# Optimization experiments

Measured on AMD Instinct MI355X. Metric: run time of the kernel, lower is better.

## Reference

```python
import jax, jax.numpy as jnp
import numpy as np

HIDDEN = 896
N_HEADS = 14
N_KV = 2
HEAD_DIM = 64
GROUPS = N_HEADS // N_KV  # 7
ROPE_THETA = 1000000.0
B, S = 2, 2048
NEG = -1e9


def rotate_half(x):
    x1 = x[..., : x.shape[-1] // 2]
    x2 = x[..., x.shape[-1] // 2:]
    return jnp.concatenate([-x2, x1], axis=-1)


def setup_inputs() -> dict:
    key = jax.random.key(0)
    ks = jax.random.split(key, 8)
    scale = 0.02
    hidden_states = jax.random.normal(ks[0], (B, S, HIDDEN), dtype=jnp.float32)
    # causal additive mask [1,1,S,S]
    causal = jnp.tril(jnp.ones((S, S), dtype=bool))
    attention_mask = jnp.where(causal, 0.0, NEG).astype(jnp.float32)[None, None]
    Wq = jax.random.normal(ks[1], (HIDDEN, N_HEADS * HEAD_DIM), dtype=jnp.float32) * scale
    bq = jnp.zeros((N_HEADS * HEAD_DIM,), dtype=jnp.float32)
    Wk = jax.random.normal(ks[2], (HIDDEN, N_KV * HEAD_DIM), dtype=jnp.float32) * scale
    bk = jnp.zeros((N_KV * HEAD_DIM,), dtype=jnp.float32)
    Wv = jax.random.normal(ks[3], (HIDDEN, N_KV * HEAD_DIM), dtype=jnp.float32) * scale
    bv = jnp.zeros((N_KV * HEAD_DIM,), dtype=jnp.float32)
    Wo = jax.random.normal(ks[4], (HIDDEN, HIDDEN), dtype=jnp.float32) * scale
    return {"hidden_states": hidden_states, "attention_mask": attention_mask,
            "Wq": Wq, "bq": bq, "Wk": Wk, "bk": bk, "Wv": Wv, "bv": bv,
            "Wo": Wo, "position_offset": 0}


def reference(hidden_states, attention_mask, Wq, bq, Wk, bk, Wv, bv, Wo, position_offset):
    batch, seq, _ = hidden_states.shape
    # QKV projections -> [B, heads, S, head_dim]
    q = (hidden_states @ Wq + bq).reshape(batch, seq, N_HEADS, HEAD_DIM).transpose(0, 2, 1, 3)
    k = (hidden_states @ Wk + bk).reshape(batch, seq, N_KV, HEAD_DIM).transpose(0, 2, 1, 3)
    v = (hidden_states @ Wv + bv).reshape(batch, seq, N_KV, HEAD_DIM).transpose(0, 2, 1, 3)
    # RoPE (computed inline from position_offset, matches precomputed cos/sin tables)
    inv_freq = 1.0 / (ROPE_THETA ** (jnp.arange(0, HEAD_DIM, 2, dtype=jnp.float32) / HEAD_DIM))
    pos = (position_offset + jnp.arange(seq)).astype(jnp.float32)  # [S]
    freqs = pos[:, None] * inv_freq[None, :]  # [S, HD/2]
    emb = jnp.concatenate([freqs, freqs], axis=-1)  # [S, HD]
    cos = jnp.cos(emb)[None, None]  # [1,1,S,HD]
    sin = jnp.sin(emb)[None, None]
    q = q * cos + rotate_half(q) * sin
    k = k * cos + rotate_half(k) * sin
    # GQA: repeat kv heads
    k = jnp.repeat(k, GROUPS, axis=1)
    v = jnp.repeat(v, GROUPS, axis=1)
    scores = jnp.einsum('bhqd,bhkd->bhqk', q, k) / jnp.sqrt(jnp.float32(HEAD_DIM))
    scores = scores + attention_mask
    weights = jax.nn.softmax(scores, axis=-1)
    out = jnp.einsum('bhqk,bhkd->bhqd', weights, v)
    out = out.transpose(0, 2, 1, 3).reshape(batch, seq, HIDDEN)
    return out @ Wo
```

## Files before the change

kernel.cpp:

```cpp
#include <hip/hip_runtime.h>
#include <stdint.h>

#define DEV __device__ __forceinline__

using bf16x8 = __attribute__((ext_vector_type(8))) short;
using f32x4  = __attribute__((ext_vector_type(4))) float;

DEV float b2f(uint16_t h){ return __uint_as_float(((uint32_t)h)<<16); }
DEV uint16_t f2b(float f){ uint32_t u=__float_as_uint(f); u += 0x7fffu + ((u>>16)&1u); return (uint16_t)(u>>16); }
DEV uint32_t pk2(float a, float b){
  return __builtin_amdgcn_perm(__float_as_uint(b), __float_as_uint(a), 0x07060302u);
}

#define GLOAD16(gp, lp) __builtin_amdgcn_global_load_lds( \
    (__attribute__((address_space(1))) void*)(gp), \
    (__attribute__((address_space(3))) void*)(lp), 16, 0, 0)

constexpr int S_    = 2048;
constexpr int HID   = 896;
constexpr int NH    = 14;
constexpr int NKV   = 2;
constexpr int HD    = 64;
constexpr int BATCH = 2;
constexpr int MROWS = BATCH * S_;
constexpr int NQKV  = 1152;
constexpr int SROWS = 1536;
constexpr int OPSTR = BATCH * NH * SROWS * 64;
constexpr int MLSTR = BATCH * NH * SROWS;
constexpr float QSCALE = 0.125f * 1.4426950408889634f;

__global__ void prep_all_kernel(const float* __restrict__ X,
                                const float* __restrict__ Wq, const float* __restrict__ Wk,
                                const float* __restrict__ Wv, const float* __restrict__ Wo,
                                const float* __restrict__ bq, const float* __restrict__ bk,
                                const float* __restrict__ bv, const int* __restrict__ pos0,
                                uint16_t* __restrict__ Xb,
                                uint16_t* __restrict__ WqkvT, uint16_t* __restrict__ WoT,
                                float* __restrict__ bqkv,
                                float* __restrict__ cosT, float* __restrict__ sinT) {
  const int blk = blockIdx.x, tid = threadIdx.x;
  if (blk < 1792) {
    const int lx = tid & 31, ly = tid >> 5;
    const float* src; uint16_t* dst; int ncols, rowOff, i;
    if (blk < 784)       { src = Wq; dst = WqkvT; ncols = 896; rowOff = 0;    i = blk;       }
    else if (blk < 896)  { src = Wk; dst = WqkvT; ncols = 128; rowOff = 896;  i = blk - 784; }
    else if (blk < 1008) { src = Wv; dst = WqkvT; ncols = 128; rowOff = 1024; i = blk - 896; }
    else                 { src = Wo; dst = WoT;   ncols = 896; rowOff = 0;    i = blk - 1008;}
    const int nb = ncols >> 5;
    const int n0 = (i % nb) * 32, k0 = (i / nb) * 32;
    __shared__ uint16_t tile[32][33];
    #pragma unroll
    for (int r = 0; r < 32; r += 8)
      tile[ly + r][lx] = f2b(src[(size_t)(k0 + ly + r) * ncols + (n0 + lx)]);
    __syncthreads();
    #pragma unroll
    for (int r = 0; r < 32; r += 8)
      dst[(size_t)(rowOff + n0 + ly + r) * 896 + (k0 + lx)] = tile[lx][ly + r];
  } else if (blk < 5376) {
    int i = (blk - 1792) * 256 + tid;
    float4 v = ((const float4*)X)[i];
    union { uint16_t u[4]; uint64_t q; } r;
    r.u[0] = f2b(v.x); r.u[1] = f2b(v.y); r.u[2] = f2b(v.z); r.u[3] = f2b(v.w);
    ((uint64_t*)Xb)[i] = r.q;
  } else if (blk < 5632) {
    int idx = (blk - 5376) * 256 + tid;
    int s = idx >> 5, j = idx & 31;
    float inv = exp2f(-(float)j * (19.931568569324174f / 32.0f));
    float ang = (float)(pos0[0] + s) * inv;
    float sv, cv;
    sincosf(ang, &sv, &cv);
    cosT[idx] = cv; sinT[idx] = sv;
  } else {
    int i = (blk - 5632) * 256 + tid;
    if (i < NQKV) bqkv[i] = i < 896 ? bq[i] : (i < 1024 ? bk[i - 896] : bv[i - 1024]);
  }
}

__global__ void packv_kernel(const uint16_t* __restrict__ Vf, uint16_t* __restrict__ Vt) {
  __shared__ uint16_t tile[64][65];
  const int s0 = blockIdx.x * 64;
  const int g  = blockIdx.y;
  const int b = g >> 1, kv = g & 1;
  const int lx = threadIdx.x & 63, ly = threadIdx.x >> 6;
  #pragma unroll
  for (int i = 0; i < 64; i += 4)
    tile[ly + i][lx] = Vf[(size_t)(b * S_ + s0 + ly + i) * 128 + kv * 64 + lx];
  __syncthreads();
  #pragma unroll
  for (int i = 0; i < 64; i += 4)
    Vt[((size_t)g * HD + ly + i) * S_ + s0 + lx] = tile[lx][ly + i];
}

template <int EPI>
__global__ __launch_bounds__(256) void gemm_bt_kernel(
    const uint16_t* __restrict__ A, const uint16_t* __restrict__ Bt,
    const float* __restrict__ bias, void* __restrict__ Cv, int N, int K,
    const float* __restrict__ cosT, const float* __restrict__ sinT,
    uint16_t* __restrict__ Qb, uint16_t* __restrict__ Kb, uint16_t* __restrict__ Vf) {
  __shared__ __align__(16) uint16_t As[128 * 64];
  __shared__ __align__(16) uint16_t Bs[64 * 64];
  const int tid = threadIdx.x;
  const int l = tid & 63, w = tid >> 6;
  const int m0 = blockIdx.x * 128, n0 = blockIdx.y * 64;
  const int wr = w * 32;

  f32x4 acc[2][4] = {};
  for (int k0 = 0; k0 < K; k0 += 64) {
    #pragma unroll
    for (int i = 0; i < 4; ++i) {
      int cid = i * 256 + tid;
      int row = cid >> 3;
      int sch = (cid & 7) ^ (row & 7);
      GLOAD16(A + (size_t)(m0 + row) * K + (k0 + sch * 8), (char*)As + cid * 16);
    }
    #pragma unroll
    for (int i = 0; i < 2; ++i) {
      int cid = i * 256 + tid;
      int row = cid >> 3;
      int sch = (cid & 7) ^ (row & 7);
      GLOAD16(Bt + (size_t)(n0 + row) * K + (k0 + sch * 8), (char*)Bs + cid * 16);
    }
    __syncthreads();
    __builtin_amdgcn_s_setprio(1);
    #pragma unroll
    for (int ks = 0; ks < 2; ++ks) {
      bf16x8 af[2], bfr[4];
      #pragma unroll
      for (int mi = 0; mi < 2; ++mi) {
        int row = wr + mi * 16 + (l & 15);
        int ch = ((l >> 4) + ks * 4) ^ (row & 7);
        af[mi] = *(const bf16x8*)((const char*)As + row * 128 + ch * 16);
      }
      #pragma unroll
      for (int ni = 0; ni < 4; ++ni) {
        int row = ni * 16 + (l & 15);
        int ch = ((l >> 4) + ks * 4) ^ (row & 7);
        bfr[ni] = *(const bf16x8*)((const char*)Bs + row * 128 + ch * 16);
      }
      #pragma unroll
      for (int mi = 0; mi < 2; ++mi)
        #pragma unroll
        for (int ni = 0; ni < 4; ++ni)
          acc[mi][ni] = __builtin_amdgcn_mfma_f32_16x16x32_bf16(af[mi], bfr[ni], acc[mi][ni], 0, 0, 0);
    }
    __builtin_amdgcn_s_setprio(0);
    __syncthreads();
  }

  const int tc = l & 15, g = l >> 4;
  if (EPI == 1) {
    if (n0 < 896) {
      #pragma unroll
      for (int mi = 0; mi < 2; ++mi) {
        #pragma unroll
        for (int jr = 0; jr < 4; ++jr) {
          int row = m0 + wr + mi * 16 + g * 4 + jr;
          int bb = row >> 11, s = row & (S_ - 1);
          const float* cp = cosT + s * 32;
          const float* sp = sinT + s * 32;
          #pragma unroll
          for (int ni = 0; ni < 2; ++ni) {
            int col = n0 + ni * 16 + tc;
            int j = col & 63;
            float c = cp[j], sn = sp[j];
            float alo = acc[mi][ni][jr] + bias[col];
            float ahi = acc[mi][ni + 2][jr] + bias[col + 32];
            size_t dst = ((size_t)(bb * NH + (n0 >> 6)) * S_ + s) * HD + j;
            Qb[dst]      = f2b((alo * c - ahi * sn) * QSCALE);
            Qb[dst + 32] = f2b((ahi * c + alo * sn) * QSCALE);
          }
        }
      }
    } else if (n0 < 1024) {
      #pragma unroll
      for (int mi = 0; mi < 2; ++mi) {
        #pragma unroll
        for (int jr = 0; jr < 4; ++jr) {
          int row = m0 + wr + mi * 16 + g * 4 + jr;
          int bb = row >> 11, s = row & (S_ - 1);
          const float* cp = cosT + s * 32;
          const float* sp = sinT + s * 32;
          #pragma unroll
          for (int ni = 0; ni < 2; ++ni) {
            int col = n0 + ni * 16 + tc;
            int j = col & 63;
            float c = cp[j], sn = sp[j];
            float alo = acc[mi][ni][jr] + bias[col];
            float ahi = acc[mi][ni + 2][jr] + bias[col + 32];
            size_t dst = ((size_t)(bb * NKV + ((n0 - 896) >> 6)) * S_ + s) * HD + j;
            Kb[dst]      = f2b(alo * c - ahi * sn);
            Kb[dst + 32] = f2b(ahi * c + alo * sn);
          }
        }
      }
    } else {
      #pragma unroll
      for (int mi = 0; mi < 2; ++mi)
        #pragma unroll
        for (int ni = 0; ni < 4; ++ni) {
          int col = n0 + ni * 16 + tc;
          #pragma unroll
          for (int jr = 0; jr < 4; ++jr) {
            int row = m0 + wr + mi * 16 + g * 4 + jr;
            Vf[(size_t)row * 128 + (col - 1024)] = f2b(acc[mi][ni][jr] + bias[col]);
          }
        }
    }
  } else {
    #pragma unroll
    for (int mi = 0; mi < 2; ++mi) {
      #pragma unroll
      for (int ni = 0; ni < 4; ++ni) {
        int col = n0 + ni * 16 + tc;
        #pragma unroll
        for (int j = 0; j < 4; ++j) {
          int row = m0 + wr + mi * 16 + g * 4 + j;
          ((float*)Cv)[(size_t)row * N + col] = acc[mi][ni][j];
        }
      }
    }
  }
}

__global__ __launch_bounds__(448) void attn_kernel(
    const uint16_t* __restrict__ Qb, const uint16_t* __restrict__ Kb,
    const uint16_t* __restrict__ Vt, uint16_t* __restrict__ Ob,
    uint16_t* __restrict__ Op, float2* __restrict__ mlp) {
  __shared__ __align__(16) uint16_t Ks[2][64 * 64];
  __shared__ __align__(16) uint16_t Vs[2][64 * 64];
  const int tid = threadIdx.x, l = tid & 63, w = tid >> 6;
  const int u = blockIdx.x;
  const int kv = blockIdx.y & 1, b = blockIdx.y >> 1;
  const int tc = l & 15, g = l >> 4;
  const int srcA = (((2 * g) & 3) << 4) | tc;
  const int srcB = (((2 * g + 1) & 3) << 4) | tc;

  int qt16, ck;
  if (u < 32)       { qt16 = u;                   ck = 0; }
  else if (u < 96)  { int i = u - 32;  qt16 = 32 + (i >> 1); ck = i & 1; }
  else if (u < 192) { int i = u - 96;  int q3 = i / 3; qt16 = 64 + q3; ck = i - 3 * q3; }
  else              { int i = u - 192; qt16 = 96 + (i >> 2); ck = i & 3; }
  const int ntiles = (qt16 >> 2) + 1;
  const int nch    = (qt16 >> 5) + 1;
  const int tlo    = 8 * ck;
  const int thi    = (8 * ck + 8 < ntiles) ? (8 * ck + 8) : ntiles;
  const int ns     = thi - tlo;
  const bool dodiag = (ck == nch - 1);
  const bool split  = (nch > 1);

  const int h  = kv * 7 + w;
  const int qg = qt16 * 16 + tc;

  const uint16_t* Khead = Kb + (size_t)(b * NKV + kv) * S_ * HD;
  const uint16_t* Vhead = Vt + (size_t)(b * NKV + kv) * HD * S_;

  auto stage = [&](int t, int bi) {
    const int t0 = t * 64;
    #pragma unroll
    for (int i = 0; i < 2; ++i) {
      if (i == 0 || tid < 64) {
        int cid = i * 448 + tid;
        int row = cid >> 3, sch = (cid & 7) ^ (row & 7);
        GLOAD16(Khead + (size_t)(t0 + row) * HD + sch * 8, (char*)Ks[bi] + cid * 16);
        GLOAD16(Vhead + (size_t)row * S_ + t0 + sch * 8,   (char*)Vs[bi] + cid * 16);
      }
    }
  };

  const uint16_t* qptr = Qb + ((size_t)(b * NH + h) * S_ + qg) * HD + g * 8;
  bf16x8 qf0 = *(const bf16x8*)qptr;
  bf16x8 qf1 = *(const bf16x8*)(qptr + 32);

  f32x4 oacc[4] = {};
  float mrow = -1e30f, lrow = 0.f;

  stage(tlo, 0);

  #pragma unroll 1
  for (int i = 0; i < ns; ++i) {
    const int t = tlo + i;
    asm volatile("s_waitcnt vmcnt(0)" ::: "memory");
    __builtin_amdgcn_s_barrier();
    if (i + 1 < ns) stage(t + 1, (i + 1) & 1);

    const uint16_t* Kc = Ks[i & 1];
    const uint16_t* Vc = Vs[i & 1];
    const int t0 = t * 64;

    f32x4 sacc[4] = {};
    __builtin_amdgcn_s_setprio(1);
    #pragma unroll
    for (int ks = 0; ks < 2; ++ks) {
      bf16x8 qf = ks ? qf1 : qf0;
      #pragma unroll
      for (int c = 0; c < 4; ++c) {
        int trow = c * 16 + tc;
        int ch = (g + ks * 4) ^ (tc & 7);
        bf16x8 kf = *(const bf16x8*)((const char*)Kc + trow * 128 + ch * 16);
        sacc[c] = __builtin_amdgcn_mfma_f32_16x16x32_bf16(kf, qf, sacc[c], 0, 0, 0);
      }
    }
    __builtin_amdgcn_s_setprio(0);

    if (dodiag && t == ntiles - 1) {
      #pragma unroll
      for (int c = 0; c < 4; ++c) {
        int kvb = t0 + c * 16 + g * 4;
        #pragma unroll
        for (int r = 0; r < 4; ++r)
          if (kvb + r > qg) sacc[c][r] = -1e30f;
      }
    }

    float pmax = sacc[0][0];
    #pragma unroll
    for (int c = 0; c < 4; ++c)
      #pragma unroll
      for (int r = 0; r < 4; ++r) pmax = fmaxf(pmax, sacc[c][r]);
    if (__any(pmax > mrow + 11.5f)) {
      float mt = fmaxf(pmax, __shfl_xor(pmax, 16));
      mt = fmaxf(mt, __shfl_xor(mt, 32));
      float mn = fmaxf(mrow, mt);
      float corr = exp2f(mrow - mn);
      mrow = mn;
      lrow *= corr;
      #pragma unroll
      for (int dt = 0; dt < 4; ++dt) oacc[dt] *= corr;
    }
    float rs = 0.f;
    #pragma unroll
    for (int c = 0; c < 4; ++c)
      #pragma unroll
      for (int r = 0; r < 4; ++r) {
        float e = exp2f(sacc[c][r] - mrow);
        sacc[c][r] = e; rs += e;
      }
    lrow += rs;

    uint32_t w0[4], w1[4];
    #pragma unroll
    for (int c = 0; c < 4; ++c) {
      w0[c] = pk2(sacc[c][0], sacc[c][1]);
      w1[c] = pk2(sacc[c][2], sacc[c][3]);
    }
    const bool lo = g < 2;
    bf16x8 pf[2];
    {
      union { uint32_t u[4]; bf16x8 v; } p0, p1;
      uint32_t a0 = __shfl((int)w0[0], srcA), a1 = __shfl((int)w1[0], srcA);
      uint32_t a2 = __shfl((int)w0[0], srcB), a3 = __shfl((int)w1[0], srcB);
      uint32_t b0 = __shfl((int)w0[1], srcA), b1 = __shfl((int)w1[1], srcA);
      uint32_t b2 = __shfl((int)w0[1], srcB), b3 = __shfl((int)w1[1], srcB);
      p0.u[0] = lo ? a0 : b0; p0.u[1] = lo ? a1 : b1;
      p0.u[2] = lo ? a2 : b2; p0.u[3] = lo ? a3 : b3;
      pf[0] = p0.v;
      uint32_t c0 = __shfl((int)w0[2], srcA), c1 = __shfl((int)w1[2], srcA);
      uint32_t c2 = __shfl((int)w0[2], srcB), c3 = __shfl((int)w1[2], srcB);
      uint32_t d0 = __shfl((int)w0[3], srcA), d1 = __shfl((int)w1[3], srcA);
      uint32_t d2 = __shfl((int)w0[3], srcB), d3 = __shfl((int)w1[3], srcB);
      p1.u[0] = lo ? c0 : d0; p1.u[1] = lo ? c1 : d1;
      p1.u[2] = lo ? c2 : d2; p1.u[3] = lo ? c3 : d3;
      pf[1] = p1.v;
    }

    __builtin_amdgcn_s_setprio(1);
    #pragma unroll
    for (int ks = 0; ks < 2; ++ks) {
      #pragma unroll
      for (int dt = 0; dt < 4; ++dt) {
        int drow = dt * 16 + tc;
        int vch = (g + ks * 4) ^ (tc & 7);
        bf16x8 vf = *(const bf16x8*)((const char*)Vc + drow * 128 + vch * 16);
        oacc[dt] = __builtin_amdgcn_mfma_f32_16x16x32_bf16(vf, pf[ks], oacc[dt], 0, 0, 0);
      }
    }
    __builtin_amdgcn_s_setprio(0);
  }

  float ltot = lrow;
  ltot += __shfl_xor(ltot, 16);
  ltot += __shfl_xor(ltot, 32);

  if (!split) {
    float inv = 1.0f / ltot;
    size_t obase = (size_t)(b * S_ + qg) * HID + h * HD;
    #pragma unroll
    for (int dt = 0; dt < 4; ++dt) {
      union { uint16_t u[4]; uint64_t q; } o;
      #pragma unroll
      for (int r = 0; r < 4; ++r) o.u[r] = f2b(oacc[dt][r] * inv);
      *(uint64_t*)(Ob + obase + dt * 16 + g * 4) = o.q;
    }
  } else {
    size_t rowid = (size_t)(b * NH + h) * SROWS + (qg - 512);
    uint16_t* Opc = Op + (size_t)ck * OPSTR + rowid * 64;
    #pragma unroll
    for (int dt = 0; dt < 4; ++dt) {
      union { uint16_t u[4]; uint64_t q; } o;
      #pragma unroll
      for (int r = 0; r < 4; ++r) o.u[r] = f2b(oacc[dt][r]);
      *(uint64_t*)(Opc + dt * 16 + g * 4) = o.q;
    }
    if (g == 0) mlp[(size_t)ck * MLSTR + rowid] = make_float2(mrow, ltot);
  }
}

__global__ void combine_kernel(const uint16_t* __restrict__ Op, const float2* __restrict__ mlp,
                               uint16_t* __restrict__ Ob) {
  int idx = blockIdx.x * 256 + threadIdx.x;
  int r = idx >> 4;
  int d0 = (idx & 15) * 4;
  int bh = r / SROWS;
  int sr = r - bh * SROWS;
  int s = 512 + sr;
  int nch = (s >> 9) + 1;
  float M = -1e30f;
  #pragma unroll 4
  for (int c = 0; c < 4; ++c)
    if (c < nch) M = fmaxf(M, mlp[(size_t)c * MLSTR + r].x);
  float den = 0.f, acc[4] = {0.f, 0.f, 0.f, 0.f};
  #pragma unroll 4
  for (int c = 0; c < 4; ++c) {
    if (c >= nch) continue;
    float2 ml = mlp[(size_t)c * MLSTR + r];
    float wg = exp2f(ml.x - M);
    den += ml.y * wg;
    union { uint16_t u[4]; uint64_t q; } o;
    o.q = *(const uint64_t*)(Op + (size_t)c * OPSTR + (size_t)r * 64 + d0);
    #pragma unroll
    for (int j = 0; j < 4; ++j) acc[j] += b2f(o.u[j]) * wg;
  }
  float inv = 1.0f / den;
  union { uint16_t u[4]; uint64_t q; } oo;
  #pragma unroll
  for (int j = 0; j < 4; ++j) oo.u[j] = f2b(acc[j] * inv);
  int bb = bh / NH, hh = bh - bb * NH;
  *(uint64_t*)(Ob + (size_t)(bb * S_ + s) * HID + hh * HD + d0) = oo.q;
}

extern "C" void kernel_launch(void* const* d_in, const int* in_sizes, int n_in,
                              void* d_out, int out_size, void* d_ws, size_t ws_size,
                              hipStream_t stream) {
  (void)in_sizes; (void)n_in; (void)out_size; (void)ws_size;
  const float* X  = (const float*)d_in[0];
  const float* Wq = (const float*)d_in[2];
  const float* bq = (const float*)d_in[3];
  const float* Wk = (const float*)d_in[4];
  const float* bk = (const float*)d_in[5];
  const float* Wv = (const float*)d_in[6];
  const float* bv = (const float*)d_in[7];
  const float* Wo = (const float*)d_in[8];
  const int* pos  = (const int*)d_in[9];

  char* p = (char*)d_ws;
  auto carve = [&](size_t n) -> char* { char* r = p; p += (n + 255) & ~(size_t)255; return r; };

  uint16_t* Xb    = (uint16_t*)carve((size_t)MROWS * HID * 2);
  uint16_t* WqkvT = (uint16_t*)carve((size_t)NQKV * 896 * 2);
  uint16_t* WoT   = (uint16_t*)carve((size_t)896 * 896 * 2);
  float*    bqkv  = (float*)carve((size_t)NQKV * 4);
  float*    cosT  = (float*)carve((size_t)S_ * 32 * 4);
  float*    sinT  = (float*)carve((size_t)S_ * 32 * 4);
  uint16_t* Qb    = (uint16_t*)carve((size_t)MROWS * HID * 2);
  uint16_t* Kb    = (uint16_t*)carve((size_t)MROWS * 128 * 2);
  uint16_t* Vf    = (uint16_t*)carve((size_t)MROWS * 128 * 2);
  uint16_t* Vt    = (uint16_t*)carve((size_t)MROWS * 128 * 2);
  uint16_t* Op    = (uint16_t*)carve((size_t)OPSTR * 4 * 2);
  float2*   mlp   = (float2*)carve((size_t)MLSTR * 4 * 8);
  uint16_t* Ob    = Xb;

  prep_all_kernel<<<dim3(5637), 256, 0, stream>>>(X, Wq, Wk, Wv, Wo, bq, bk, bv, pos,
                                                  Xb, WqkvT, WoT, bqkv, cosT, sinT);

  gemm_bt_kernel<1><<<dim3(MROWS / 128, NQKV / 64), 256, 0, stream>>>(
      Xb, WqkvT, bqkv, nullptr, NQKV, 896, cosT, sinT, Qb, Kb, Vf);

  packv_kernel<<<dim3(S_ / 64, BATCH * NKV), 256, 0, stream>>>(Vf, Vt);

  attn_kernel<<<dim3(320, NKV * BATCH), 448, 0, stream>>>(Qb, Kb, Vt, Ob, Op, mlp);
  combine_kernel<<<dim3(BATCH * NH * SROWS * 16 / 256), 256, 0, stream>>>(Op, mlp, Ob);

  gemm_bt_kernel<0><<<dim3(MROWS / 128, 896 / 64), 256, 0, stream>>>(
      Ob, WoT, nullptr, d_out, 896, 896, nullptr, nullptr, nullptr, nullptr, nullptr);
}
```

Baseline: 99.63 us.

## Double-buffer GEMM LDS tiles and use raw v_exp_f32 in softmax

The projection GEMM now keeps two LDS buffers and prefetches the next K tile with global_load_lds while the MFMAs consume the current one, leaving one barrier per iteration instead of two. This aims to hide global-load latency behind compute, at the cost of double the LDS footprint, which may lower occupancy. Separately, exp2f calls in the attention and combine kernels are swapped for inline-asm v_exp_f32. That drops the denormal and range handling exp2f wraps around the instruction, at some risk of different behaviour for very negative arguments.

```diff
diff --git a/kernel.cpp b/kernel.cpp
--- a/kernel.cpp
+++ b/kernel.cpp
@@ -11,6 +11,7 @@
 DEV uint32_t pk2(float a, float b){
   return __builtin_amdgcn_perm(__float_as_uint(b), __float_as_uint(a), 0x07060302u);
 }
+DEV float fexp2(float x){ float r; asm("v_exp_f32 %0, %1" : "=v"(r) : "v"(x)); return r; }
 
 #define GLOAD16(gp, lp) __builtin_amdgcn_global_load_lds( \
     (__attribute__((address_space(1))) void*)(gp), \
@@ -97,30 +98,41 @@
     const float* __restrict__ bias, void* __restrict__ Cv, int N, int K,
     const float* __restrict__ cosT, const float* __restrict__ sinT,
     uint16_t* __restrict__ Qb, uint16_t* __restrict__ Kb, uint16_t* __restrict__ Vf) {
-  __shared__ __align__(16) uint16_t As[128 * 64];
-  __shared__ __align__(16) uint16_t Bs[64 * 64];
+  __shared__ __align__(16) uint16_t As[2][128 * 64];
+  __shared__ __align__(16) uint16_t Bs[2][64 * 64];
   const int tid = threadIdx.x;
   const int l = tid & 63, w = tid >> 6;
   const int m0 = blockIdx.x * 128, n0 = blockIdx.y * 64;
   const int wr = w * 32;
 
-  f32x4 acc[2][4] = {};
-  for (int k0 = 0; k0 < K; k0 += 64) {
+  auto stage = [&](int k0, int bi) {
     #pragma unroll
     for (int i = 0; i < 4; ++i) {
       int cid = i * 256 + tid;
       int row = cid >> 3;
       int sch = (cid & 7) ^ (row & 7);
-      GLOAD16(A + (size_t)(m0 + row) * K + (k0 + sch * 8), (char*)As + cid * 16);
+      GLOAD16(A + (size_t)(m0 + row) * K + (k0 + sch * 8), (char*)As[bi] + cid * 16);
     }
     #pragma unroll
     for (int i = 0; i < 2; ++i) {
       int cid = i * 256 + tid;
       int row = cid >> 3;
       int sch = (cid & 7) ^ (row & 7);
-      GLOAD16(Bt + (size_t)(n0 + row) * K + (k0 + sch * 8), (char*)Bs + cid * 16);
-    }
-    __syncthreads();
+      GLOAD16(Bt + (size_t)(n0 + row) * K + (k0 + sch * 8), (char*)Bs[bi] + cid * 16);
+    }
+  };
+
+  const int nk = K >> 6;
+  f32x4 acc[2][4] = {};
+  stage(0, 0);
+  asm volatile("s_waitcnt vmcnt(0)" ::: "memory");
+  __builtin_amdgcn_s_barrier();
+
+  #pragma unroll 1
+  for (int t = 0; t < nk; ++t) {
+    if (t + 1 < nk) stage((t + 1) << 6, (t + 1) & 1);
+    const uint16_t* Ac = As[t & 1];
+    const uint16_t* Bc = Bs[t & 1];
     __builtin_amdgcn_s_setprio(1);
     #pragma unroll
     for (int ks = 0; ks < 2; ++ks) {
@@ -129,13 +141,13 @@
       for (int mi = 0; mi < 2; ++mi) {
         int row = wr + mi * 16 + (l & 15);
         int ch = ((l >> 4) + ks * 4) ^ (row & 7);
-        af[mi] = *(const bf16x8*)((const char*)As + row * 128 + ch * 16);
+        af[mi] = *(const bf16x8*)((const char*)Ac + row * 128 + ch * 16);
       }
       #pragma unroll
       for (int ni = 0; ni < 4; ++ni) {
         int row = ni * 16 + (l & 15);
         int ch = ((l >> 4) + ks * 4) ^ (row & 7);
-        bfr[ni] = *(const bf16x8*)((const char*)Bs + row * 128 + ch * 16);
+        bfr[ni] = *(const bf16x8*)((const char*)Bc + row * 128 + ch * 16);
       }
       #pragma unroll
       for (int mi = 0; mi < 2; ++mi)
@@ -144,7 +156,8 @@
           acc[mi][ni] = __builtin_amdgcn_mfma_f32_16x16x32_bf16(af[mi], bfr[ni], acc[mi][ni], 0, 0, 0);
     }
     __builtin_amdgcn_s_setprio(0);
-    __syncthreads();
+    asm volatile("s_waitcnt vmcnt(0)" ::: "memory");
+    __builtin_amdgcn_s_barrier();
   }
 
   const int tc = l & 15, g = l >> 4;
@@ -321,7 +334,7 @@
       float mt = fmaxf(pmax, __shfl_xor(pmax, 16));
       mt = fmaxf(mt, __shfl_xor(mt, 32));
       float mn = fmaxf(mrow, mt);
-      float corr = exp2f(mrow - mn);
+      float corr = fexp2(mrow - mn);
       mrow = mn;
       lrow *= corr;
       #pragma unroll
@@ -332,7 +345,7 @@
     for (int c = 0; c < 4; ++c)
       #pragma unroll
       for (int r = 0; r < 4; ++r) {
-        float e = exp2f(sacc[c][r] - mrow);
+        float e = fexp2(sacc[c][r] - mrow);
         sacc[c][r] = e; rs += e;
       }
     lrow += rs;
@@ -423,7 +436,7 @@
   for (int c = 0; c < 4; ++c) {
     if (c >= nch) continue;
     float2 ml = mlp[(size_t)c * MLSTR + r];
-    float wg = exp2f(ml.x - M);
+    float wg = fexp2(ml.x - M);
     den += ml.y * wg;
     union { uint16_t u[4]; uint64_t q; } o;
     o.q = *(const uint64_t*)(Op + (size_t)c * OPSTR + (size_t)r * 64 + d0);
```

New measurement: 93.91 us. 5.7% less time.
